# Performance work log

Hardware: AMD Instinct MI355X
Metric: run time of the kernel (lower is better)

The kernel has to match this reference:

```python
import jax, jax.numpy as jnp
import numpy as np

B, S, C, H, L = 8, 1000, 512, 8, 6
D = C // H  # 64


def setup_inputs() -> dict:
    key = jax.random.key(0)
    ks = jax.random.split(key, 6)
    s = 0.02
    x = jax.random.normal(ks[0], (B, S, C), dtype=jnp.float32)
    ln_g = jnp.ones((L, C), jnp.float32)
    ln_b = jnp.zeros((L, C), jnp.float32)
    Wq = jax.random.normal(ks[1], (L, C, C), jnp.float32) * s
    Wk = jax.random.normal(ks[2], (L, C, C), jnp.float32) * s
    Wv = jax.random.normal(ks[3], (L, C, C), jnp.float32) * s
    Wo = jax.random.normal(ks[4], (L, C, C), jnp.float32) * s
    bq = jnp.zeros((L, C), jnp.float32)
    bk = jnp.zeros((L, C), jnp.float32)
    bv = jnp.zeros((L, C), jnp.float32)
    bo = jnp.zeros((L, C), jnp.float32)
    return dict(x=x, ln_g=ln_g, ln_b=ln_b, Wq=Wq, bq=bq, Wk=Wk, bk=bk,
                Wv=Wv, bv=bv, Wo=Wo, bo=bo)


def _layer_norm(x, g, b, eps=1e-5):
    m = jnp.mean(x, axis=-1, keepdims=True)
    v = jnp.mean(jnp.square(x - m), axis=-1, keepdims=True)
    return (x - m) * jax.lax.rsqrt(v + eps) * g + b


def reference(x, ln_g, ln_b, Wq, bq, Wk, bk, Wv, bv, Wo, bo):
    # First streaming call: history is empty, so q = k = v = x for every
    # layer (x is never updated between layers); only the last layer's
    # output is returned. Mask is all-ones (no-op); dropout is eval-mode.
    Bn, Sn, Cn = x.shape
    scale = 1.0 / np.sqrt(D).astype(np.float32)
    # additive relative-position bias: pos[i, j] = i - j
    pos = (jnp.arange(Sn)[:, None] - jnp.arange(Sn)[None, :]).astype(x.dtype)
    out = x
    for i in range(L):
        xn = _layer_norm(x, ln_g[i], ln_b[i])  # same LN for q, k, v
        q = (xn @ Wq[i].T + bq[i]).reshape(Bn, Sn, H, D)
        k = (xn @ Wk[i].T + bk[i]).reshape(Bn, Sn, H, D)
        v = (xn @ Wv[i].T + bv[i]).reshape(Bn, Sn, H, D)
        scores = jnp.einsum('bqhd,bkhd->bhqk', q, k) * scale + pos  # [B,H,S,S]
        attn = jax.nn.softmax(scores, axis=-1)
        ctx = jnp.einsum('bhqk,bkhd->bqhd', attn, v).reshape(Bn, Sn, Cn)
        out = ctx @ Wo[i].T + bo[i]
    return out
```

## Files before the change

### kernel.cpp

```cpp
#include <hip/hip_runtime.h>
#include <math.h>


typedef __bf16 bf16x8 __attribute__((ext_vector_type(8)));
typedef __bf16 bf16x4 __attribute__((ext_vector_type(4)));
typedef float f32x4 __attribute__((ext_vector_type(4)));

__device__ __forceinline__ void async16(const __bf16* g, __bf16* l) {
  __builtin_amdgcn_global_load_lds((const __attribute__((address_space(1))) void*)g,
                                   (__attribute__((address_space(3))) void*)l, 16, 0, 0);
}

__global__ __launch_bounds__(256) void prep_k(const float* __restrict__ Wq, const float* __restrict__ Wk,
                                              const float* __restrict__ Wv, const float* __restrict__ Wo,
                                              __bf16* __restrict__ wdst,
                                              const float* __restrict__ x, const float* __restrict__ lg,
                                              const float* __restrict__ lb, __bf16* __restrict__ y) {
  const int bid = blockIdx.x;
  if (bid < 1024) {
    const float* src = (bid < 256) ? Wq : (bid < 512) ? Wk : (bid < 768) ? Wv : Wo;
    int idx = ((bid & 255) * 256 + threadIdx.x) * 4;
    float4 v = *(const float4*)(src + idx);
    bf16x4 o = {(__bf16)v.x, (__bf16)v.y, (__bf16)v.z, (__bf16)v.w};
    *(bf16x4*)(wdst + (size_t)(bid >> 8) * 262144 + idx) = o;
    return;
  }
  const int row = (bid - 1024) * 4 + (threadIdx.x >> 6);
  const int l = threadIdx.x & 63;
  const float* xr = x + (size_t)row * 512 + l * 8;
  float4 a = *(const float4*)xr, c = *(const float4*)(xr + 4);
  float s = a.x + a.y + a.z + a.w + c.x + c.y + c.z + c.w;
#pragma unroll
  for (int m = 1; m < 64; m <<= 1) s += __shfl_xor(s, m, 64);
  float mean = s * (1.0f / 512.0f);
  float d[8] = {a.x - mean, a.y - mean, a.z - mean, a.w - mean,
                c.x - mean, c.y - mean, c.z - mean, c.w - mean};
  float qq = 0.f;
#pragma unroll
  for (int e = 0; e < 8; ++e) qq += d[e] * d[e];
#pragma unroll
  for (int m = 1; m < 64; m <<= 1) qq += __shfl_xor(qq, m, 64);
  float rstd = rsqrtf(qq * (1.0f / 512.0f) + 1e-5f);
  float4 g0 = *(const float4*)(lg + l * 8), g1 = *(const float4*)(lg + l * 8 + 4);
  float4 b0 = *(const float4*)(lb + l * 8), b1 = *(const float4*)(lb + l * 8 + 4);
  float gg[8] = {g0.x, g0.y, g0.z, g0.w, g1.x, g1.y, g1.z, g1.w};
  float bb[8] = {b0.x, b0.y, b0.z, b0.w, b1.x, b1.y, b1.z, b1.w};
  bf16x8 o;
#pragma unroll
  for (int e = 0; e < 8; ++e) o[e] = (__bf16)(d[e] * rstd * gg[e] + bb[e]);
  *(bf16x8*)(y + (size_t)row * 512 + l * 8) = o;
}

template <int PROJ>
__global__ __launch_bounds__(256) void gemm_k(const __bf16* __restrict__ A,
                                              const __bf16* __restrict__ Wq_,
                                              const __bf16* __restrict__ Wkv_,
                                              const float* __restrict__ bq_,
                                              const float* __restrict__ bk_,
                                              const float* __restrict__ bv_,
                                              void* __restrict__ Yq_,
                                              __bf16* __restrict__ Ykv_) {
  __shared__ __align__(16) __bf16 Ws[64 * 512];
  const int t = threadIdx.x, w = t >> 6, l = t & 63, g = l >> 4, l15 = l & 15;
  const int id = blockIdx.x;

  const __bf16* Ab;
  const __bf16* Wt;
  const float* bp;
  int maxrow, ldY;
  void* Yp;
  if (PROJ || id < 256) {
    int low3 = id & 7, rest = id >> 3;
    int n = rest & 7, m = (rest >> 3) * 8 + low3;
    Ab = A + (size_t)m * 256 * 512;
    maxrow = 8000 - m * 256; if (maxrow > 256) maxrow = 256;
    Wt = Wq_ + (size_t)n * 64 * 512;
    bp = bq_ + n * 64;
    ldY = 512;
    if (PROJ) Yp = (float*)Yq_ + (size_t)m * 256 * 512 + n * 64;
    else      Yp = (__bf16*)Yq_ + (size_t)m * 256 * 512 + n * 64;
  } else {
    int kid = id - 256;
    int b = kid & 7, n = kid >> 3;
    Ab = A + (size_t)b * 1000 * 512;
    maxrow = 128;
    Wt = Wkv_ + (size_t)n * 64 * 512;
    int nc = n * 64;
    bp = (nc < 512) ? (bk_ + nc) : (bv_ + (nc - 512));
    ldY = 1024;
    Yp = Ykv_ + (size_t)b * 128 * 1024 + nc;
  }

  float bias_j[4];
#pragma unroll
  for (int j = 0; j < 4; ++j) bias_j[j] = bp[j * 16 + l15];

  const __bf16* ap[4];
#pragma unroll
  for (int s = 0; s < 4; ++s) {
    int r = w * 64 + s * 16 + l15;
    int cr = (r < maxrow) ? r : (maxrow - 1);
    ap[s] = Ab + (size_t)cr * 512 + g * 8;
  }
  bf16x8 abuf[2][4];
#pragma unroll
  for (int s = 0; s < 4; ++s) abuf[0][s] = *(const bf16x8*)(ap[s]);
#pragma unroll
  for (int s = 0; s < 4; ++s) abuf[1][s] = *(const bf16x8*)(ap[s] + 32);

#pragma unroll
  for (int i = 0; i < 16; ++i) {
    int s = i * 256 + t;
    int row = s >> 6, u = s & 63;
    async16(Wt + (size_t)row * 512 + ((u ^ (row & 7)) << 3), &Ws[s * 8]);
  }
  __syncthreads();

  f32x4 acc[4][4] = {};
#pragma unroll
  for (int ks = 0; ks < 16; ++ks) {
    bf16x8 ca[4];
#pragma unroll
    for (int s = 0; s < 4; ++s) ca[s] = abuf[ks & 1][s];
    if (ks < 14) {
#pragma unroll
      for (int s = 0; s < 4; ++s) abuf[ks & 1][s] = *(const bf16x8*)(ap[s] + (ks + 2) * 32);
    }
    bf16x8 bfr[4];
#pragma unroll
    for (int j = 0; j < 4; ++j) {
      int rb = j * 16 + l15;
      int u = ks * 4 + g;
      bfr[j] = *(const bf16x8*)&Ws[rb * 512 + ((u ^ (rb & 7)) << 3)];
    }
#pragma unroll
    for (int s = 0; s < 4; ++s)
#pragma unroll
      for (int j = 0; j < 4; ++j)
        acc[s][j] = __builtin_amdgcn_mfma_f32_16x16x32_bf16(ca[s], bfr[j], acc[s][j], 0, 0, 0);
  }

#pragma unroll
  for (int s = 0; s < 4; ++s)
#pragma unroll
    for (int r = 0; r < 4; ++r) {
      int lrow = w * 64 + s * 16 + g * 4 + r;
      if (lrow < maxrow) {
#pragma unroll
        for (int j = 0; j < 4; ++j) {
          float val = acc[s][j][r] + bias_j[j];
          if (PROJ) ((float*)Yp)[(size_t)lrow * ldY + j * 16 + l15] = val;
          else      ((__bf16*)Yp)[(size_t)lrow * ldY + j * 16 + l15] = (__bf16)val;
        }
      }
    }
}

__global__ __launch_bounds__(256) void attn_mfma(const __bf16* __restrict__ q,
                                                 const __bf16* __restrict__ kv,
                                                 __bf16* __restrict__ ctx) {
  __shared__ __align__(16) __bf16 Ks[128 * 64];
  __shared__ __align__(16) __bf16 Vt[64 * 128];
  __shared__ __align__(16) __bf16 Ps[4][16 * 136];
  const int t = threadIdx.x, w = t >> 6, l = t & 63, g = l >> 4, l15 = l & 15;
  const int id = blockIdx.x;
  const int low3 = id & 7, rest = id >> 3;
  const int q0 = (rest & 15) * 64;
  const int bh = (rest >> 4) * 8 + low3;
  const int b = bh >> 3, h = bh & 7;

#pragma unroll
  for (int i = 0; i < 4; ++i) {
    int s = i * 256 + t;
    int row = s >> 3, u = s & 7;
    async16(kv + (size_t)(b * 128 + row) * 1024 + h * 64 + ((u ^ (row & 7)) << 3), &Ks[s * 8]);
  }
  {
    int vrow = t & 127, dbase = (t >> 7) * 32;
    const __bf16* vp = kv + (size_t)(b * 128 + vrow) * 1024 + 512 + h * 64 + dbase;
#pragma unroll
    for (int c = 0; c < 4; ++c) {
      bf16x8 vv = *(const bf16x8*)(vp + c * 8);
#pragma unroll
      for (int e = 0; e < 8; ++e) {
        int d = dbase + c * 8 + e;
        Vt[d * 128 + (((vrow >> 3) ^ (d & 7)) << 3) + (vrow & 7)] = vv[e];
      }
    }
  }
  bf16x8 aq[2];
  {
    int qr = q0 + w * 16 + l15; if (qr > 999) qr = 999;
    const __bf16* qp = q + ((size_t)(b * 1000 + qr)) * 512 + h * 64;
    aq[0] = *(const bf16x8*)(qp + g * 8);
    aq[1] = *(const bf16x8*)(qp + 32 + g * 8);
  }
  __syncthreads();

  f32x4 ct[8] = {};
#pragma unroll
  for (int c = 0; c < 2; ++c)
#pragma unroll
    for (int nt = 0; nt < 8; ++nt) {
      int rn = nt * 16 + l15;
      bf16x8 bk = *(const bf16x8*)&Ks[rn * 64 + (((c * 4 + g) ^ (rn & 7)) << 3)];
      ct[nt] = __builtin_amdgcn_mfma_f32_16x16x32_bf16(aq[c], bk, ct[nt], 0, 0, 0);
    }

  float rs[4] = {0.f, 0.f, 0.f, 0.f};
#pragma unroll
  for (int nt = 0; nt < 8; ++nt) {
    int kg = nt * 16 + l15;
#pragma unroll
    for (int r = 0; r < 4; ++r) {
      float p = __expf(ct[nt][r] * 0.125f - (float)kg - 2.0f);
      __bf16 pb = (__bf16)p;
      Ps[w][(g * 4 + r) * 136 + kg] = pb;
      rs[r] += (float)pb;
    }
  }
#pragma unroll
  for (int r = 0; r < 4; ++r) {
    float s = rs[r];
    s += __shfl_xor(s, 1, 16);
    s += __shfl_xor(s, 2, 16);
    s += __shfl_xor(s, 4, 16);
    s += __shfl_xor(s, 8, 16);
    rs[r] = 1.0f / s;
  }

  f32x4 co[4] = {};
  bf16x8 ap[4];
#pragma unroll
  for (int c = 0; c < 4; ++c) ap[c] = *(const bf16x8*)&Ps[w][l15 * 136 + c * 32 + g * 8];
#pragma unroll
  for (int nt = 0; nt < 4; ++nt) {
    int d = nt * 16 + l15;
#pragma unroll
    for (int c = 0; c < 4; ++c) {
      bf16x8 bv = *(const bf16x8*)&Vt[d * 128 + (((c * 4 + g) ^ (d & 7)) << 3)];
      co[nt] = __builtin_amdgcn_mfma_f32_16x16x32_bf16(ap[c], bv, co[nt], 0, 0, 0);
    }
  }

#pragma unroll
  for (int r = 0; r < 4; ++r) {
    int qg = q0 + w * 16 + g * 4 + r;
    if (qg < 1000) {
      __bf16* op = ctx + ((size_t)(b * 1000 + qg)) * 512 + h * 64 + l15;
#pragma unroll
      for (int nt = 0; nt < 4; ++nt) op[nt * 16] = (__bf16)(co[nt][r] * rs[r]);
    }
  }
}

extern "C" void kernel_launch(void* const* d_in, const int* in_sizes, int n_in,
                              void* d_out, int out_size, void* d_ws, size_t ws_size,
                              hipStream_t stream) {
  const float* x    = (const float*)d_in[0];
  const float* ln_g = (const float*)d_in[1];
  const float* ln_b = (const float*)d_in[2];
  const float* Wq   = (const float*)d_in[3];
  const float* bq   = (const float*)d_in[4];
  const float* Wk   = (const float*)d_in[5];
  const float* bk   = (const float*)d_in[6];
  const float* Wv   = (const float*)d_in[7];
  const float* bv   = (const float*)d_in[8];
  const float* Wo   = (const float*)d_in[9];
  const float* bo   = (const float*)d_in[10];
  float* out = (float*)d_out;
  __bf16* ws = (__bf16*)d_ws;

  __bf16* xn  = ws;
  __bf16* q   = ws + 4096000;
  __bf16* kvb = ws + 8192000;
  __bf16* wqb = ws + 9240576;
  __bf16* wkv = wqb + 262144;
  __bf16* wob = wqb + 786432;
  __bf16* ctx = xn;

  const size_t LW = (size_t)5 * 512 * 512;
  const size_t LB = (size_t)5 * 512;

  prep_k<<<3024, 256, 0, stream>>>(Wq + LW, Wk + LW, Wv + LW, Wo + LW, wqb,
                                   x, ln_g + LB, ln_b + LB, xn);
  gemm_k<0><<<384, 256, 0, stream>>>(xn, wqb, wkv, bq + LB, bk + LB, bv + LB, q, kvb);
  attn_mfma<<<1024, 256, 0, stream>>>(q, kvb, ctx);
  gemm_k<1><<<256, 256, 0, stream>>>(ctx, wob, nullptr, bo + LB, nullptr, nullptr, out, nullptr);
}
```

Measured before the change: 142.6 us.

## Fuse prep, projections, attention and output GEMM into one cooperative kernel

Replaces the four separate launches (weight/LayerNorm prep, QKV GEMM, attention, output GEMM) with a single persistent cooperative kernel of 512 blocks. The stages are separated by grid-wide syncs, and each stage is a loop over work units. GEMM tiles shrink from 256 to 128 rows so every block gets a unit, and ctx gets its own buffer instead of aliasing xn. The aim is to remove launch gaps and tail effects between kernels, at the cost of grid-sync overhead, a fixed 64KB shared-memory footprint per block and a two-blocks-per-CU occupancy cap.

```diff
diff --git a/kernel.cpp b/kernel.cpp
--- a/kernel.cpp
+++ b/kernel.cpp
@@ -1,113 +1,44 @@
 #include <hip/hip_runtime.h>
+#include <hip/hip_cooperative_groups.h>
 #include <math.h>
 
+
+namespace cg = cooperative_groups;
 
 typedef __bf16 bf16x8 __attribute__((ext_vector_type(8)));
 typedef __bf16 bf16x4 __attribute__((ext_vector_type(4)));
 typedef float f32x4 __attribute__((ext_vector_type(4)));
 
+#define NBLK 512
+
 __device__ __forceinline__ void async16(const __bf16* g, __bf16* l) {
   __builtin_amdgcn_global_load_lds((const __attribute__((address_space(1))) void*)g,
                                    (__attribute__((address_space(3))) void*)l, 16, 0, 0);
 }
 
-__global__ __launch_bounds__(256) void prep_k(const float* __restrict__ Wq, const float* __restrict__ Wk,
-                                              const float* __restrict__ Wv, const float* __restrict__ Wo,
-                                              __bf16* __restrict__ wdst,
-                                              const float* __restrict__ x, const float* __restrict__ lg,
-                                              const float* __restrict__ lb, __bf16* __restrict__ y) {
-  const int bid = blockIdx.x;
-  if (bid < 1024) {
-    const float* src = (bid < 256) ? Wq : (bid < 512) ? Wk : (bid < 768) ? Wv : Wo;
-    int idx = ((bid & 255) * 256 + threadIdx.x) * 4;
-    float4 v = *(const float4*)(src + idx);
-    bf16x4 o = {(__bf16)v.x, (__bf16)v.y, (__bf16)v.z, (__bf16)v.w};
-    *(bf16x4*)(wdst + (size_t)(bid >> 8) * 262144 + idx) = o;
-    return;
-  }
-  const int row = (bid - 1024) * 4 + (threadIdx.x >> 6);
-  const int l = threadIdx.x & 63;
-  const float* xr = x + (size_t)row * 512 + l * 8;
-  float4 a = *(const float4*)xr, c = *(const float4*)(xr + 4);
-  float s = a.x + a.y + a.z + a.w + c.x + c.y + c.z + c.w;
-#pragma unroll
-  for (int m = 1; m < 64; m <<= 1) s += __shfl_xor(s, m, 64);
-  float mean = s * (1.0f / 512.0f);
-  float d[8] = {a.x - mean, a.y - mean, a.z - mean, a.w - mean,
-                c.x - mean, c.y - mean, c.z - mean, c.w - mean};
-  float qq = 0.f;
-#pragma unroll
-  for (int e = 0; e < 8; ++e) qq += d[e] * d[e];
-#pragma unroll
-  for (int m = 1; m < 64; m <<= 1) qq += __shfl_xor(qq, m, 64);
-  float rstd = rsqrtf(qq * (1.0f / 512.0f) + 1e-5f);
-  float4 g0 = *(const float4*)(lg + l * 8), g1 = *(const float4*)(lg + l * 8 + 4);
-  float4 b0 = *(const float4*)(lb + l * 8), b1 = *(const float4*)(lb + l * 8 + 4);
-  float gg[8] = {g0.x, g0.y, g0.z, g0.w, g1.x, g1.y, g1.z, g1.w};
-  float bb[8] = {b0.x, b0.y, b0.z, b0.w, b1.x, b1.y, b1.z, b1.w};
-  bf16x8 o;
-#pragma unroll
-  for (int e = 0; e < 8; ++e) o[e] = (__bf16)(d[e] * rstd * gg[e] + bb[e]);
-  *(bf16x8*)(y + (size_t)row * 512 + l * 8) = o;
-}
-
-template <int PROJ>
-__global__ __launch_bounds__(256) void gemm_k(const __bf16* __restrict__ A,
-                                              const __bf16* __restrict__ Wq_,
-                                              const __bf16* __restrict__ Wkv_,
-                                              const float* __restrict__ bq_,
-                                              const float* __restrict__ bk_,
-                                              const float* __restrict__ bv_,
-                                              void* __restrict__ Yq_,
-                                              __bf16* __restrict__ Ykv_) {
-  __shared__ __align__(16) __bf16 Ws[64 * 512];
-  const int t = threadIdx.x, w = t >> 6, l = t & 63, g = l >> 4, l15 = l & 15;
-  const int id = blockIdx.x;
-
-  const __bf16* Ab;
-  const __bf16* Wt;
-  const float* bp;
-  int maxrow, ldY;
-  void* Yp;
-  if (PROJ || id < 256) {
-    int low3 = id & 7, rest = id >> 3;
-    int n = rest & 7, m = (rest >> 3) * 8 + low3;
-    Ab = A + (size_t)m * 256 * 512;
-    maxrow = 8000 - m * 256; if (maxrow > 256) maxrow = 256;
-    Wt = Wq_ + (size_t)n * 64 * 512;
-    bp = bq_ + n * 64;
-    ldY = 512;
-    if (PROJ) Yp = (float*)Yq_ + (size_t)m * 256 * 512 + n * 64;
-    else      Yp = (__bf16*)Yq_ + (size_t)m * 256 * 512 + n * 64;
-  } else {
-    int kid = id - 256;
-    int b = kid & 7, n = kid >> 3;
-    Ab = A + (size_t)b * 1000 * 512;
-    maxrow = 128;
-    Wt = Wkv_ + (size_t)n * 64 * 512;
-    int nc = n * 64;
-    bp = (nc < 512) ? (bk_ + nc) : (bv_ + (nc - 512));
-    ldY = 1024;
-    Yp = Ykv_ + (size_t)b * 128 * 1024 + nc;
-  }
-
+__device__ __forceinline__ void gemm_unit(const __bf16* __restrict__ Ab, int maxrow,
+                                          const __bf16* __restrict__ Wt,
+                                          const float* __restrict__ bp,
+                                          void* __restrict__ Yp, int ldY, bool out32,
+                                          __bf16* Ws, int t) {
+  const int w = t >> 6, l = t & 63, g = l >> 4, l15 = l & 15;
   float bias_j[4];
 #pragma unroll
   for (int j = 0; j < 4; ++j) bias_j[j] = bp[j * 16 + l15];
-
-  const __bf16* ap[4];
-#pragma unroll
-  for (int s = 0; s < 4; ++s) {
-    int r = w * 64 + s * 16 + l15;
+  const __bf16* ap[2];
+#pragma unroll
+  for (int s = 0; s < 2; ++s) {
+    int r = w * 32 + s * 16 + l15;
     int cr = (r < maxrow) ? r : (maxrow - 1);
     ap[s] = Ab + (size_t)cr * 512 + g * 8;
   }
-  bf16x8 abuf[2][4];
-#pragma unroll
-  for (int s = 0; s < 4; ++s) abuf[0][s] = *(const bf16x8*)(ap[s]);
-#pragma unroll
-  for (int s = 0; s < 4; ++s) abuf[1][s] = *(const bf16x8*)(ap[s] + 32);
-
+  bf16x8 abuf[2][2];
+#pragma unroll
+  for (int s = 0; s < 2; ++s) abuf[0][s] = *(const bf16x8*)(ap[s]);
+#pragma unroll
+  for (int s = 0; s < 2; ++s) abuf[1][s] = *(const bf16x8*)(ap[s] + 32);
+
+  __syncthreads();
 #pragma unroll
   for (int i = 0; i < 16; ++i) {
     int s = i * 256 + t;
@@ -116,59 +47,57 @@
   }
   __syncthreads();
 
-  f32x4 acc[4][4] = {};
+  f32x4 acc[2][4] = {};
 #pragma unroll
   for (int ks = 0; ks < 16; ++ks) {
-    bf16x8 ca[4];
-#pragma unroll
-    for (int s = 0; s < 4; ++s) ca[s] = abuf[ks & 1][s];
+    bf16x8 ca[2];
+#pragma unroll
+    for (int s = 0; s < 2; ++s) ca[s] = abuf[ks & 1][s];
     if (ks < 14) {
 #pragma unroll
-      for (int s = 0; s < 4; ++s) abuf[ks & 1][s] = *(const bf16x8*)(ap[s] + (ks + 2) * 32);
+      for (int s = 0; s < 2; ++s) abuf[ks & 1][s] = *(const bf16x8*)(ap[s] + (ks + 2) * 32);
     }
     bf16x8 bfr[4];
 #pragma unroll
     for (int j = 0; j < 4; ++j) {
       int rb = j * 16 + l15;
-      int u = ks * 4 + g;
-      bfr[j] = *(const bf16x8*)&Ws[rb * 512 + ((u ^ (rb & 7)) << 3)];
-    }
-#pragma unroll
-    for (int s = 0; s < 4; ++s)
+      bfr[j] = *(const bf16x8*)&Ws[rb * 512 + (((ks * 4 + g) ^ (rb & 7)) << 3)];
+    }
+#pragma unroll
+    for (int s = 0; s < 2; ++s)
 #pragma unroll
       for (int j = 0; j < 4; ++j)
         acc[s][j] = __builtin_amdgcn_mfma_f32_16x16x32_bf16(ca[s], bfr[j], acc[s][j], 0, 0, 0);
   }
-
-#pragma unroll
-  for (int s = 0; s < 4; ++s)
+#pragma unroll
+  for (int s = 0; s < 2; ++s)
 #pragma unroll
     for (int r = 0; r < 4; ++r) {
-      int lrow = w * 64 + s * 16 + g * 4 + r;
+      int lrow = w * 32 + s * 16 + g * 4 + r;
       if (lrow < maxrow) {
 #pragma unroll
         for (int j = 0; j < 4; ++j) {
           float val = acc[s][j][r] + bias_j[j];
-          if (PROJ) ((float*)Yp)[(size_t)lrow * ldY + j * 16 + l15] = val;
-          else      ((__bf16*)Yp)[(size_t)lrow * ldY + j * 16 + l15] = (__bf16)val;
+          if (out32) ((float*)Yp)[(size_t)lrow * ldY + j * 16 + l15] = val;
+          else       ((__bf16*)Yp)[(size_t)lrow * ldY + j * 16 + l15] = (__bf16)val;
         }
       }
     }
 }
 
-__global__ __launch_bounds__(256) void attn_mfma(const __bf16* __restrict__ q,
-                                                 const __bf16* __restrict__ kv,
-                                                 __bf16* __restrict__ ctx) {
-  __shared__ __align__(16) __bf16 Ks[128 * 64];
-  __shared__ __align__(16) __bf16 Vt[64 * 128];
-  __shared__ __align__(16) __bf16 Ps[4][16 * 136];
-  const int t = threadIdx.x, w = t >> 6, l = t & 63, g = l >> 4, l15 = l & 15;
-  const int id = blockIdx.x;
+__device__ __forceinline__ void attn_unit(int id, const __bf16* __restrict__ q,
+                                          const __bf16* __restrict__ kv,
+                                          __bf16* __restrict__ ctx, char* smem, int t) {
+  __bf16* Ks = (__bf16*)smem;
+  __bf16* Vt = (__bf16*)(smem + 16384);
+  __bf16* Ps = (__bf16*)(smem + 32768);
+  const int w = t >> 6, l = t & 63, g = l >> 4, l15 = l & 15;
   const int low3 = id & 7, rest = id >> 3;
   const int q0 = (rest & 15) * 64;
   const int bh = (rest >> 4) * 8 + low3;
   const int b = bh >> 3, h = bh & 7;
 
+  __syncthreads();
 #pragma unroll
   for (int i = 0; i < 4; ++i) {
     int s = i * 256 + t;
@@ -215,7 +144,7 @@
     for (int r = 0; r < 4; ++r) {
       float p = __expf(ct[nt][r] * 0.125f - (float)kg - 2.0f);
       __bf16 pb = (__bf16)p;
-      Ps[w][(g * 4 + r) * 136 + kg] = pb;
+      Ps[w * 2176 + (g * 4 + r) * 136 + kg] = pb;
       rs[r] += (float)pb;
     }
   }
@@ -230,19 +159,18 @@
   }
 
   f32x4 co[4] = {};
-  bf16x8 ap[4];
-#pragma unroll
-  for (int c = 0; c < 4; ++c) ap[c] = *(const bf16x8*)&Ps[w][l15 * 136 + c * 32 + g * 8];
+  bf16x8 app[4];
+#pragma unroll
+  for (int c = 0; c < 4; ++c) app[c] = *(const bf16x8*)&Ps[w * 2176 + l15 * 136 + c * 32 + g * 8];
 #pragma unroll
   for (int nt = 0; nt < 4; ++nt) {
     int d = nt * 16 + l15;
 #pragma unroll
     for (int c = 0; c < 4; ++c) {
       bf16x8 bv = *(const bf16x8*)&Vt[d * 128 + (((c * 4 + g) ^ (d & 7)) << 3)];
-      co[nt] = __builtin_amdgcn_mfma_f32_16x16x32_bf16(ap[c], bv, co[nt], 0, 0, 0);
-    }
-  }
-
+      co[nt] = __builtin_amdgcn_mfma_f32_16x16x32_bf16(app[c], bv, co[nt], 0, 0, 0);
+    }
+  }
 #pragma unroll
   for (int r = 0; r < 4; ++r) {
     int qg = q0 + w * 16 + g * 4 + r;
@@ -250,6 +178,92 @@
       __bf16* op = ctx + ((size_t)(b * 1000 + qg)) * 512 + h * 64 + l15;
 #pragma unroll
       for (int nt = 0; nt < 4; ++nt) op[nt * 16] = (__bf16)(co[nt][r] * rs[r]);
+    }
+  }
+}
+
+__global__ __launch_bounds__(256, 2) void mega_k(
+    const float* __restrict__ x, const float* __restrict__ lg, const float* __restrict__ lb,
+    const float* __restrict__ Wq, const float* __restrict__ Wk,
+    const float* __restrict__ Wv, const float* __restrict__ Wo,
+    const float* __restrict__ bq, const float* __restrict__ bk,
+    const float* __restrict__ bv, const float* __restrict__ bo,
+    __bf16* __restrict__ xn, __bf16* __restrict__ q, __bf16* __restrict__ kvb,
+    __bf16* __restrict__ wall, __bf16* __restrict__ ctx,
+    float* __restrict__ out) {
+  __shared__ __align__(16) char smem[65536];
+  cg::grid_group grid = cg::this_grid();
+  const int t = threadIdx.x, bid = blockIdx.x;
+  const int w = t >> 6, l = t & 63;
+
+  {
+    const float* srcs[4] = {Wq, Wk, Wv, Wo};
+#pragma unroll
+    for (int it = 0; it < 2; ++it) {
+      int mat = it * 2 + (bid >> 8);
+      int off = (((bid & 255) * 256 + t) << 2);
+      float4 v = *(const float4*)(srcs[mat] + off);
+      bf16x4 o = {(__bf16)v.x, (__bf16)v.y, (__bf16)v.z, (__bf16)v.w};
+      *(bf16x4*)(wall + (size_t)mat * 262144 + off) = o;
+    }
+#pragma unroll
+    for (int it = 0; it < 4; ++it) {
+      int row = it * 2048 + bid * 4 + w;
+      if (row < 8000) {
+        const float* xr = x + (size_t)row * 512 + l * 8;
+        float4 a = *(const float4*)xr, c = *(const float4*)(xr + 4);
+        float s = a.x + a.y + a.z + a.w + c.x + c.y + c.z + c.w;
+#pragma unroll
+        for (int m = 1; m < 64; m <<= 1) s += __shfl_xor(s, m, 64);
+        float mean = s * (1.0f / 512.0f);
+        float d[8] = {a.x - mean, a.y - mean, a.z - mean, a.w - mean,
+                      c.x - mean, c.y - mean, c.z - mean, c.w - mean};
+        float qq = 0.f;
+#pragma unroll
+        for (int e = 0; e < 8; ++e) qq += d[e] * d[e];
+#pragma unroll
+        for (int m = 1; m < 64; m <<= 1) qq += __shfl_xor(qq, m, 64);
+        float rstd = rsqrtf(qq * (1.0f / 512.0f) + 1e-5f);
+        float4 g0 = *(const float4*)(lg + l * 8), g1 = *(const float4*)(lg + l * 8 + 4);
+        float4 b0 = *(const float4*)(lb + l * 8), b1 = *(const float4*)(lb + l * 8 + 4);
+        float gg[8] = {g0.x, g0.y, g0.z, g0.w, g1.x, g1.y, g1.z, g1.w};
+        float bb[8] = {b0.x, b0.y, b0.z, b0.w, b1.x, b1.y, b1.z, b1.w};
+        bf16x8 o;
+#pragma unroll
+        for (int e = 0; e < 8; ++e) o[e] = (__bf16)(d[e] * rstd * gg[e] + bb[e]);
+        *(bf16x8*)(xn + (size_t)row * 512 + l * 8) = o;
+      }
+    }
+  }
+  grid.sync();
+
+  {
+    int low3 = bid & 7, n = (bid >> 3) & 7, mq = ((bid >> 6) << 3) + low3;
+    if (mq < 63) {
+      int mr = 8000 - mq * 128; if (mr > 128) mr = 128;
+      gemm_unit(xn + (size_t)mq * 128 * 512, mr, wall + (size_t)n * 64 * 512, bq + n * 64,
+                q + (size_t)mq * 128 * 512 + n * 64, 512, false, (__bf16*)smem, t);
+    }
+    if (bid < 128) {
+      int b = bid & 7, nk = bid >> 3;
+      int nc = nk * 64;
+      const float* bp = (nc < 512) ? (bk + nc) : (bv + (nc - 512));
+      gemm_unit(xn + (size_t)b * 1000 * 512, 128, wall + 262144 + (size_t)nk * 64 * 512, bp,
+                kvb + (size_t)b * 128 * 1024 + nc, 1024, false, (__bf16*)smem, t);
+    }
+  }
+  grid.sync();
+
+#pragma unroll
+  for (int i = 0; i < 2; ++i) attn_unit(i * NBLK + bid, q, kvb, ctx, smem, t);
+  grid.sync();
+
+  {
+    int low3 = bid & 7, n = (bid >> 3) & 7, mq = ((bid >> 6) << 3) + low3;
+    if (mq < 63) {
+      int mr = 8000 - mq * 128; if (mr > 128) mr = 128;
+      gemm_unit(ctx + (size_t)mq * 128 * 512, mr, wall + 786432 + (size_t)n * 64 * 512, bo + n * 64,
+                out + (size_t)mq * 128 * 512 + n * 64, 512, true, (__bf16*)smem, t);
     }
   }
 }
@@ -271,20 +285,31 @@
   float* out = (float*)d_out;
   __bf16* ws = (__bf16*)d_ws;
 
-  __bf16* xn  = ws;
-  __bf16* q   = ws + 4096000;
-  __bf16* kvb = ws + 8192000;
-  __bf16* wqb = ws + 9240576;
-  __bf16* wkv = wqb + 262144;
-  __bf16* wob = wqb + 786432;
-  __bf16* ctx = xn;
+  __bf16* xn   = ws;
+  __bf16* q    = ws + 4096000;
+  __bf16* kvb  = ws + 8192000;
+  __bf16* wall = ws + 9240576;
+  __bf16* ctx  = ws + 10289152;
 
   const size_t LW = (size_t)5 * 512 * 512;
   const size_t LB = (size_t)5 * 512;
 
-  prep_k<<<3024, 256, 0, stream>>>(Wq + LW, Wk + LW, Wv + LW, Wo + LW, wqb,
-                                   x, ln_g + LB, ln_b + LB, xn);
-  gemm_k<0><<<384, 256, 0, stream>>>(xn, wqb, wkv, bq + LB, bk + LB, bv + LB, q, kvb);
-  attn_mfma<<<1024, 256, 0, stream>>>(q, kvb, ctx);
-  gemm_k<1><<<256, 256, 0, stream>>>(ctx, wob, nullptr, bo + LB, nullptr, nullptr, out, nullptr);
-}
+  const float* xg  = x;
+  const float* lgp = ln_g + LB;
+  const float* lbp = ln_b + LB;
+  const float* wqp = Wq + LW;
+  const float* wkp = Wk + LW;
+  const float* wvp = Wv + LW;
+  const float* wop = Wo + LW;
+  const float* bqp = bq + LB;
+  const float* bkp = bk + LB;
+  const float* bvp = bv + LB;
+  const float* bop = bo + LB;
+
+  void* args[] = {(void*)&xg, (void*)&lgp, (void*)&lbp,
+                  (void*)&wqp, (void*)&wkp, (void*)&wvp, (void*)&wop,
+                  (void*)&bqp, (void*)&bkp, (void*)&bvp, (void*)&bop,
+                  (void*)&xn, (void*)&q, (void*)&kvb, (void*)&wall, (void*)&ctx,
+                  (void*)&out};
+  hipLaunchCooperativeKernel((void*)mega_k, dim3(NBLK), dim3(256), args, 0, stream);
+}
```

Measured after the change: 344.2 us. 2.41x slower.
